# Performance work log

Measured on AMD Instinct MI355X. Metric: run time of the kernel, lower is better.

## Reference

```python
import jax, jax.numpy as jnp
import numpy as np

EMBED_DIM = 1024
NUM_HEADS = 16
HEAD_DIM = EMBED_DIM // NUM_HEADS


def layer_norm(x, gamma, beta, eps=1e-5):
    mu = jnp.mean(x, axis=-1, keepdims=True)
    var = jnp.var(x, axis=-1, keepdims=True)
    return (x - mu) * jax.lax.rsqrt(var + eps) * gamma + beta


def setup_inputs() -> dict:
    key = jax.random.key(0)
    ks = jax.random.split(key, 8)
    D = EMBED_DIM
    s = 1.0 / np.sqrt(D)
    x = jax.random.normal(ks[0], (2, 2048, D), dtype=jnp.float32)
    Wq = jax.random.uniform(ks[1], (D, D), jnp.float32, -s, s)
    Wk = jax.random.uniform(ks[2], (D, D), jnp.float32, -s, s)
    Wv = jax.random.uniform(ks[3], (D, D), jnp.float32, -s, s)
    W1 = jax.random.uniform(ks[4], (D, 4 * D), jnp.float32, -s, s)
    b1 = jnp.zeros((4 * D,), jnp.float32)
    W2 = jax.random.uniform(ks[5], (4 * D, D), jnp.float32, -1.0 / np.sqrt(4 * D), 1.0 / np.sqrt(4 * D))
    b2 = jnp.zeros((D,), jnp.float32)
    g1 = jnp.ones((D,), jnp.float32); be1 = jnp.zeros((D,), jnp.float32)
    g2 = jnp.ones((D,), jnp.float32); be2 = jnp.zeros((D,), jnp.float32)
    return {"x": x, "Wq": Wq, "Wk": Wk, "Wv": Wv, "W1": W1, "b1": b1,
            "W2": W2, "b2": b2, "g1": g1, "be1": be1, "g2": g2, "be2": be2}


def reference(x, Wq, Wk, Wv, W1, b1, W2, b2, g1, be1, g2, be2):
    B, S, D = x.shape
    H, Hd = NUM_HEADS, HEAD_DIM
    x_norm = layer_norm(x, g1, be1)
    # QKV projections (no bias), split into heads: [B, H, S, Hd]
    q = (x_norm @ Wq).reshape(B, S, H, Hd).transpose(0, 2, 1, 3)
    k = (x_norm @ Wk).reshape(B, S, H, Hd).transpose(0, 2, 1, 3)
    v = (x_norm @ Wv).reshape(B, S, H, Hd).transpose(0, 2, 1, 3)
    energy = jnp.einsum('bhqd,bhkd->bhqk', q, k)
    attn = jax.nn.softmax(energy / jnp.sqrt(jnp.float32(Hd)), axis=-1)
    out = jnp.einsum('bhqk,bhkd->bhqd', attn, v)
    attention = out.transpose(0, 2, 1, 3).reshape(B, S, D)
    x_res = attention + x
    x_norm2 = layer_norm(x_res, g2, be2)
    # Faithful quirk: FFN applied to x_res (not x_norm2)
    ffn_out = jax.nn.relu(x_res @ W1 + b1) @ W2 + b2
    return ffn_out + x_norm2
```

## Files before the change

kernel.cpp:

```cpp
#include <hip/hip_runtime.h>
#include <hip/hip_bf16.h>
#include <stdint.h>

typedef __hip_bfloat16 bf16;
typedef __attribute__((ext_vector_type(4))) float f32x4;
typedef __attribute__((ext_vector_type(8))) short s16x8;
typedef __attribute__((ext_vector_type(4))) short s16x4;

#define DEV static __device__ __forceinline__

DEV short f2bf(float f) {
  bf16 h = __float2bfloat16(f);
  short s;
  __builtin_memcpy(&s, &h, 2);
  return s;
}
DEV float bf2f(short s) {
  bf16 h;
  __builtin_memcpy(&h, &s, 2);
  return __bfloat162float(h);
}

__global__ __launch_bounds__(256) void transpose_cvt(
    const float* __restrict__ W, bf16* __restrict__ Wt, int K, int N)
{
  __shared__ float tile[32][33];
  const int n0 = blockIdx.x << 5;
  const int k0 = blockIdx.y << 5;
  const int tx = threadIdx.x & 31, ty = threadIdx.x >> 5;
#pragma unroll
  for (int i = 0; i < 4; ++i)
    tile[ty + i * 8][tx] = W[(size_t)(k0 + ty + i * 8) * N + n0 + tx];
  __syncthreads();
#pragma unroll
  for (int i = 0; i < 4; ++i)
    Wt[(size_t)(n0 + ty + i * 8) * K + k0 + tx] = __float2bfloat16(tile[tx][ty + i * 8]);
}

__global__ __launch_bounds__(256) void ln_bf16(
    const float* __restrict__ x, const float* __restrict__ g,
    const float* __restrict__ be, bf16* __restrict__ out)
{
  const int t = threadIdx.x;
  const size_t row = blockIdx.x;
  const float4 v = ((const float4*)(x + row * 1024))[t];
  float s = v.x + v.y + v.z + v.w;
  float ss = v.x * v.x + v.y * v.y + v.z * v.z + v.w * v.w;
#pragma unroll
  for (int off = 32; off > 0; off >>= 1) {
    s += __shfl_down(s, off);
    ss += __shfl_down(ss, off);
  }
  __shared__ float sh[8];
  const int wave = t >> 6, lane = t & 63;
  if (!lane) { sh[wave] = s; sh[4 + wave] = ss; }
  __syncthreads();
  s = sh[0] + sh[1] + sh[2] + sh[3];
  ss = sh[4] + sh[5] + sh[6] + sh[7];
  const float mean = s * (1.f / 1024.f);
  const float rstd = rsqrtf(ss * (1.f / 1024.f) - mean * mean + 1e-5f);
  const float4 gv = ((const float4*)g)[t];
  const float4 bv = ((const float4*)be)[t];
  s16x4 o;
  o[0] = f2bf((v.x - mean) * rstd * gv.x + bv.x);
  o[1] = f2bf((v.y - mean) * rstd * gv.y + bv.y);
  o[2] = f2bf((v.z - mean) * rstd * gv.z + bv.z);
  o[3] = f2bf((v.w - mean) * rstd * gv.w + bv.w);
  ((s16x4*)(out + row * 1024))[t] = o;
}

__global__ __launch_bounds__(256) void add_ln_bf16(
    const float* __restrict__ a, const float* __restrict__ x,
    const float* __restrict__ g, const float* __restrict__ be,
    bf16* __restrict__ xres, bf16* __restrict__ xnorm)
{
  const int t = threadIdx.x;
  const size_t row = blockIdx.x;
  const float4 av = ((const float4*)(a + row * 1024))[t];
  const float4 xv = ((const float4*)(x + row * 1024))[t];
  float4 v;
  v.x = av.x + xv.x; v.y = av.y + xv.y; v.z = av.z + xv.z; v.w = av.w + xv.w;
  float s = v.x + v.y + v.z + v.w;
  float ss = v.x * v.x + v.y * v.y + v.z * v.z + v.w * v.w;
#pragma unroll
  for (int off = 32; off > 0; off >>= 1) {
    s += __shfl_down(s, off);
    ss += __shfl_down(ss, off);
  }
  __shared__ float sh[8];
  const int wave = t >> 6, lane = t & 63;
  if (!lane) { sh[wave] = s; sh[4 + wave] = ss; }
  __syncthreads();
  s = sh[0] + sh[1] + sh[2] + sh[3];
  ss = sh[4] + sh[5] + sh[6] + sh[7];
  const float mean = s * (1.f / 1024.f);
  const float rstd = rsqrtf(ss * (1.f / 1024.f) - mean * mean + 1e-5f);
  const float4 gv = ((const float4*)g)[t];
  const float4 bv = ((const float4*)be)[t];
  s16x4 r, o;
  r[0] = f2bf(v.x); r[1] = f2bf(v.y); r[2] = f2bf(v.z); r[3] = f2bf(v.w);
  o[0] = f2bf((v.x - mean) * rstd * gv.x + bv.x);
  o[1] = f2bf((v.y - mean) * rstd * gv.y + bv.y);
  o[2] = f2bf((v.z - mean) * rstd * gv.z + bv.z);
  o[3] = f2bf((v.w - mean) * rstd * gv.w + bv.w);
  ((s16x4*)(xres + row * 1024))[t] = r;
  ((s16x4*)(xnorm + row * 1024))[t] = o;
}

__global__ __launch_bounds__(256) void ffn2_epi(
    const float* __restrict__ p0, float* __restrict__ out,
    const float* __restrict__ bias, const bf16* __restrict__ xn2)
{
  const int t = threadIdx.x;
  const size_t row = blockIdx.x;
  const float4 a = ((const float4*)(p0 + row * 1024))[t];
  const float4 b = ((const float4*)(out + row * 1024))[t];
  const float4 bv = ((const float4*)bias)[t];
  const s16x4 xv = ((const s16x4*)(xn2 + row * 1024))[t];
  float4 o;
  o.x = a.x + b.x + bv.x + bf2f(xv[0]);
  o.y = a.y + b.y + bv.y + bf2f(xv[1]);
  o.z = a.z + b.z + bv.z + bf2f(xv[2]);
  o.w = a.w + b.w + bv.w + bf2f(xv[3]);
  ((float4*)(out + row * 1024))[t] = o;
}

template <int EPI>
__global__ __launch_bounds__(256) void gemm_bt(
    const bf16* __restrict__ A, const bf16* __restrict__ Bt,
    void* __restrict__ C, const float* __restrict__ bias,
    const bf16* __restrict__ add_bf16, int M, int N, int K)
{
  __shared__ bf16 sA0[128 * 64];
  __shared__ bf16 sB0[128 * 64];
  __shared__ bf16 sA1[128 * 64];
  __shared__ bf16 sB1[128 * 64];
  const int tid = threadIdx.x;
  const int wave = tid >> 6, lane = tid & 63;
  const int fr = lane & 15, fg = lane >> 4;
  const int f7 = fr & 7;
  const int wr = wave >> 1, wc = wave & 1;
  const int nbx = N >> 7;
  int bid = blockIdx.x;
  if ((gridDim.x & 7) == 0) {
    const int cpx = gridDim.x >> 3;
    bid = (bid & 7) * cpx + (bid >> 3);
  }
  const int brow = (bid / nbx) << 7;
  const int bcol = (bid % nbx) << 7;

  f32x4 acc[4][4] = {};

  const int rsub = lane >> 3;
  const int cl = (lane & 7) ^ rsub;
  size_t ga[4], gb[4];
  int la[4];
#pragma unroll
  for (int j = 0; j < 4; ++j) {
    const int r = wave * 32 + j * 8;
    ga[j] = (size_t)(brow + r + rsub) * K + cl * 8;
    gb[j] = (size_t)(bcol + r + rsub) * K + cl * 8;
    la[j] = r * 64;
  }

#define GSTAGE(SA, SB, koff)                                                   \
  do {                                                                         \
    _Pragma("unroll")                                                          \
    for (int jj = 0; jj < 4; ++jj) {                                           \
      __builtin_amdgcn_global_load_lds(                                        \
          (const __attribute__((address_space(1))) uint32_t*)(A + ga[jj] + (koff)), \
          (__attribute__((address_space(3))) uint32_t*)(&SA[la[jj]]), 16, 0, 0);  \
      __builtin_amdgcn_global_load_lds(                                        \
          (const __attribute__((address_space(1))) uint32_t*)(Bt + gb[jj] + (koff)),\
          (__attribute__((address_space(3))) uint32_t*)(&SB[la[jj]]), 16, 0, 0);  \
    }                                                                          \
  } while (0)

#define COMPUTE(SA, SB)                                                        \
  do {                                                                         \
    s16x8 af[4][2], bfr[4][2];                                                 \
    _Pragma("unroll")                                                          \
    for (int m = 0; m < 4; ++m)                                                \
      _Pragma("unroll")                                                        \
      for (int kk = 0; kk < 2; ++kk)                                           \
        af[m][kk] = *(const s16x8*)(&SA[(wr * 64 + m * 16 + fr) * 64 +         \
                                        (((kk * 4 + fg) ^ f7) << 3)]);         \
    _Pragma("unroll")                                                          \
    for (int n = 0; n < 4; ++n)                                                \
      _Pragma("unroll")                                                        \
      for (int kk = 0; kk < 2; ++kk)                                           \
        bfr[n][kk] = *(const s16x8*)(&SB[(wc * 64 + n * 16 + fr) * 64 +        \
                                         (((kk * 4 + fg) ^ f7) << 3)]);        \
    _Pragma("unroll")                                                          \
    for (int kk = 0; kk < 2; ++kk)                                             \
      _Pragma("unroll")                                                        \
      for (int m = 0; m < 4; ++m)                                              \
        _Pragma("unroll")                                                      \
        for (int n = 0; n < 4; ++n)                                            \
          acc[m][n] = __builtin_amdgcn_mfma_f32_16x16x32_bf16(                 \
              af[m][kk], bfr[n][kk], acc[m][n], 0, 0, 0);                      \
  } while (0)

  GSTAGE(sA0, sB0, 0);
  __syncthreads();

  int kt = 0;
  for (;;) {
    if (kt + 64 < K) {
      GSTAGE(sA1, sB1, kt + 64);
      COMPUTE(sA0, sB0);
      __syncthreads();
    } else {
      COMPUTE(sA0, sB0);
      break;
    }
    kt += 64;
    if (kt + 64 < K) {
      GSTAGE(sA0, sB0, kt + 64);
      COMPUTE(sA1, sB1);
      __syncthreads();
    } else {
      COMPUTE(sA1, sB1);
      break;
    }
    kt += 64;
  }
#undef GSTAGE
#undef COMPUTE

  const int crow = brow + wr * 64;
  const int ccol = bcol + wc * 64;
#pragma unroll
  for (int m = 0; m < 4; ++m) {
#pragma unroll
    for (int n = 0; n < 4; ++n) {
      const int col = ccol + n * 16 + fr;
#pragma unroll
      for (int j = 0; j < 4; ++j) {
        const int row = crow + m * 16 + fg * 4 + j;
        float v = acc[m][n][j];
        if (EPI == 0) {
          ((bf16*)C)[(size_t)row * N + col] = __float2bfloat16(v);
        } else if (EPI == 1) {
          v += bias[col];
          v = fmaxf(v, 0.f);
          ((bf16*)C)[(size_t)row * N + col] = __float2bfloat16(v);
        } else {
          float a;
          {
            bf16 hb = add_bf16[(size_t)row * N + col];
            a = __bfloat162float(hb);
          }
          ((float*)C)[(size_t)row * N + col] = v + bias[col] + a;
        }
      }
    }
  }
}

__global__ __launch_bounds__(256) void gemm_splitk(
    const bf16* __restrict__ A, const bf16* __restrict__ Bt,
    float* __restrict__ P0, float* __restrict__ P1, int M, int N, int K, int KH)
{
  __shared__ bf16 sA0[128 * 64];
  __shared__ bf16 sB0[128 * 64];
  __shared__ bf16 sA1[128 * 64];
  __shared__ bf16 sB1[128 * 64];
  const int tid = threadIdx.x;
  const int wave = tid >> 6, lane = tid & 63;
  const int fr = lane & 15, fg = lane >> 4;
  const int f7 = fr & 7;
  const int wr = wave >> 1, wc = wave & 1;
  const int nbx = N >> 7;
  int bid = blockIdx.x;
  if ((gridDim.x & 7) == 0) {
    const int cpx = gridDim.x >> 3;
    bid = (bid & 7) * cpx + (bid >> 3);
  }
  const int brow = (bid / nbx) << 7;
  const int bcol = (bid % nbx) << 7;
  const int kbeg = blockIdx.y * KH;
  float* Cp = blockIdx.y ? P1 : P0;

  f32x4 acc[4][4] = {};

  const int rsub = lane >> 3;
  const int cl = (lane & 7) ^ rsub;
  size_t ga[4], gb[4];
  int la[4];
#pragma unroll
  for (int j = 0; j < 4; ++j) {
    const int r = wave * 32 + j * 8;
    ga[j] = (size_t)(brow + r + rsub) * K + cl * 8 + kbeg;
    gb[j] = (size_t)(bcol + r + rsub) * K + cl * 8 + kbeg;
    la[j] = r * 64;
  }

#define GSTAGE(SA, SB, koff)                                                   \
  do {                                                                         \
    _Pragma("unroll")                                                          \
    for (int jj = 0; jj < 4; ++jj) {                                           \
      __builtin_amdgcn_global_load_lds(                                        \
          (const __attribute__((address_space(1))) uint32_t*)(A + ga[jj] + (koff)), \
          (__attribute__((address_space(3))) uint32_t*)(&SA[la[jj]]), 16, 0, 0);  \
      __builtin_amdgcn_global_load_lds(                                        \
          (const __attribute__((address_space(1))) uint32_t*)(Bt + gb[jj] + (koff)),\
          (__attribute__((address_space(3))) uint32_t*)(&SB[la[jj]]), 16, 0, 0);  \
    }                                                                          \
  } while (0)

#define COMPUTE(SA, SB)                                                        \
  do {                                                                         \
    s16x8 af[4][2], bfr[4][2];                                                 \
    _Pragma("unroll")                                                          \
    for (int m = 0; m < 4; ++m)                                                \
      _Pragma("unroll")                                                        \
      for (int kk = 0; kk < 2; ++kk)                                           \
        af[m][kk] = *(const s16x8*)(&SA[(wr * 64 + m * 16 + fr) * 64 +         \
                                        (((kk * 4 + fg) ^ f7) << 3)]);         \
    _Pragma("unroll")                                                          \
    for (int n = 0; n < 4; ++n)                                                \
      _Pragma("unroll")                                                        \
      for (int kk = 0; kk < 2; ++kk)                                           \
        bfr[n][kk] = *(const s16x8*)(&SB[(wc * 64 + n * 16 + fr) * 64 +        \
                                         (((kk * 4 + fg) ^ f7) << 3)]);        \
    _Pragma("unroll")                                                          \
    for (int kk = 0; kk < 2; ++kk)                                             \
      _Pragma("unroll")                                                        \
      for (int m = 0; m < 4; ++m)                                              \
        _Pragma("unroll")                                                      \
        for (int n = 0; n < 4; ++n)                                            \
          acc[m][n] = __builtin_amdgcn_mfma_f32_16x16x32_bf16(                 \
              af[m][kk], bfr[n][kk], acc[m][n], 0, 0, 0);                      \
  } while (0)

  GSTAGE(sA0, sB0, 0);
  __syncthreads();

  int kt = 0;
  for (;;) {
    if (kt + 64 < KH) {
      GSTAGE(sA1, sB1, kt + 64);
      COMPUTE(sA0, sB0);
      __syncthreads();
    } else {
      COMPUTE(sA0, sB0);
      break;
    }
    kt += 64;
    if (kt + 64 < KH) {
      GSTAGE(sA0, sB0, kt + 64);
      COMPUTE(sA1, sB1);
      __syncthreads();
    } else {
      COMPUTE(sA1, sB1);
      break;
    }
    kt += 64;
  }
#undef GSTAGE
#undef COMPUTE

  const int crow = brow + wr * 64;
  const int ccol = bcol + wc * 64;
#pragma unroll
  for (int m = 0; m < 4; ++m) {
#pragma unroll
    for (int n = 0; n < 4; ++n) {
      const int col = ccol + n * 16 + fr;
#pragma unroll
      for (int j = 0; j < 4; ++j) {
        const int row = crow + m * 16 + fg * 4 + j;
        Cp[(size_t)row * N + col] = acc[m][n][j];
      }
    }
  }
}

template <int EPI>
__global__ __launch_bounds__(512) void gemm256_bt(
    const bf16* __restrict__ A, const bf16* __restrict__ Bt,
    void* __restrict__ C, const float* __restrict__ bias, int M, int N, int K)
{
  __shared__ bf16 sA0[256 * 64];
  __shared__ bf16 sB0[256 * 64];
  __shared__ bf16 sA1[256 * 64];
  __shared__ bf16 sB1[256 * 64];
  const int tid = threadIdx.x;
  const int wave = tid >> 6, lane = tid & 63;
  const int fr = lane & 15, fg = lane >> 4;
  const int f7 = fr & 7;
  const int wr = wave >> 2, wc = wave & 3;
  const int nbx = N >> 8;
  int bid = blockIdx.x;
  if ((gridDim.x & 7) == 0) {
    const int cpx = gridDim.x >> 3;
    bid = (bid & 7) * cpx + (bid >> 3);
  }
  const int brow = (bid / nbx) << 8;
  const int bcol = (bid % nbx) << 8;

  f32x4 acc[8][4] = {};

  const int rsub = lane >> 3;
  const int cl = (lane & 7) ^ rsub;
  size_t ga[4], gb[4];
  int la[4];
#pragma unroll
  for (int j = 0; j < 4; ++j) {
    const int r = j * 64 + wave * 8;
    ga[j] = (size_t)(brow + r + rsub) * K + cl * 8;
    gb[j] = (size_t)(bcol + r + rsub) * K + cl * 8;
    la[j] = r * 64;
  }

#define STG6(SA, SB, koff)                                                     \
  do {                                                                         \
    _Pragma("unroll")                                                          \
    for (int jj = 0; jj < 4; ++jj) {                                           \
      __builtin_amdgcn_global_load_lds(                                        \
          (const __attribute__((address_space(1))) uint32_t*)(A + ga[jj] + (koff)), \
          (__attribute__((address_space(3))) uint32_t*)(&SA[la[jj]]), 16, 0, 0);  \
      __builtin_amdgcn_global_load_lds(                                        \
          (const __attribute__((address_space(1))) uint32_t*)(Bt + gb[jj] + (koff)),\
          (__attribute__((address_space(3))) uint32_t*)(&SB[la[jj]]), 16, 0, 0);  \
    }                                                                          \
  } while (0)

#define CMP6(SA, SB)                                                           \
  do {                                                                         \
    s16x8 bfr[4][2];                                                           \
    _Pragma("unroll")                                                          \
    for (int n = 0; n < 4; ++n)                                                \
      _Pragma("unroll")                                                        \
      for (int kk = 0; kk < 2; ++kk)                                           \
        bfr[n][kk] = *(const s16x8*)(&SB[(wc * 64 + n * 16 + fr) * 64 +        \
                                         (((kk * 4 + fg) ^ f7) << 3)]);        \
    __builtin_amdgcn_s_setprio(1);                                             \
    _Pragma("unroll")                                                          \
    for (int m = 0; m < 8; ++m) {                                              \
      s16x8 afm[2];                                                            \
      _Pragma("unroll")                                                        \
      for (int kk = 0; kk < 2; ++kk)                                           \
        afm[kk] = *(const s16x8*)(&SA[(wr * 128 + m * 16 + fr) * 64 +          \
                                      (((kk * 4 + fg) ^ f7) << 3)]);           \
      _Pragma("unroll")                                                        \
      for (int kk = 0; kk < 2; ++kk)                                           \
        _Pragma("unroll")                                                      \
        for (int n = 0; n < 4; ++n)                                            \
          acc[m][n] = __builtin_amdgcn_mfma_f32_16x16x32_bf16(                 \
              afm[kk], bfr[n][kk], acc[m][n], 0, 0, 0);                        \
    }                                                                          \
    __builtin_amdgcn_s_setprio(0);                                             \
  } while (0)

  STG6(sA0, sB0, 0);

  int kt = 0;
  for (;;) {
    if (kt + 64 < K) {
      STG6(sA1, sB1, kt + 64);
      asm volatile("s_waitcnt vmcnt(8)" ::: "memory");
    } else {
      asm volatile("s_waitcnt vmcnt(0)" ::: "memory");
    }
    __builtin_amdgcn_s_barrier();
    __builtin_amdgcn_sched_barrier(0);
    CMP6(sA0, sB0);
    if (kt + 64 >= K) break;
    __builtin_amdgcn_s_barrier();
    __builtin_amdgcn_sched_barrier(0);
    kt += 64;
    if (kt + 64 < K) {
      STG6(sA0, sB0, kt + 64);
      asm volatile("s_waitcnt vmcnt(8)" ::: "memory");
    } else {
      asm volatile("s_waitcnt vmcnt(0)" ::: "memory");
    }
    __builtin_amdgcn_s_barrier();
    __builtin_amdgcn_sched_barrier(0);
    CMP6(sA1, sB1);
    if (kt + 64 >= K) break;
    __builtin_amdgcn_s_barrier();
    __builtin_amdgcn_sched_barrier(0);
    kt += 64;
  }
#undef STG6
#undef CMP6

  const int crow = brow + wr * 128;
  const int ccol = bcol + wc * 64;
#pragma unroll
  for (int m = 0; m < 8; ++m) {
#pragma unroll
    for (int n = 0; n < 4; ++n) {
      const int col = ccol + n * 16 + fr;
#pragma unroll
      for (int j = 0; j < 4; ++j) {
        const int row = crow + m * 16 + fg * 4 + j;
        float v = acc[m][n][j];
        if (EPI == 0) {
          ((bf16*)C)[(size_t)row * N + col] = __float2bfloat16(v);
        } else {
          v += bias[col];
          v = fmaxf(v, 0.f);
          ((bf16*)C)[(size_t)row * N + col] = __float2bfloat16(v);
        }
      }
    }
  }
}

__global__ __launch_bounds__(512, 4) void attn_fwd(
    const bf16* __restrict__ QK, const bf16* __restrict__ Vt,
    float* __restrict__ Out)
{
  const int LDK = 2048;
  const int qt = blockIdx.x;
  const int bh = blockIdx.y;
  const int b = bh >> 4, h = bh & 15;
  const int tid = threadIdx.x;
  const int wave = tid >> 6, lane = tid & 63;
  const int fr = lane & 15, fg = lane >> 4;
  const int f7 = fr & 7;

  const short* base = (const short*)QK + (size_t)b * 2048 * LDK;
  const short* Qp = base + h * 64;
  const short* Kp = base + 1024 + h * 64;
  const short* Vp = (const short*)Vt + (size_t)h * 64 * 4096 + b * 2048;
  const int q0 = qt * 128 + wave * 16;

  __shared__ short Kbuf0[64 * 64];
  __shared__ short Vbuf0[64 * 64];
  __shared__ short Kbuf1[64 * 64];
  __shared__ short Vbuf1[64 * 64];
  __shared__ short P_lds[8][16 * 72];
  short* Pw = P_lds[wave];

  const int rsub = lane >> 3;
  const int clog = (lane & 7) ^ rsub;
  const short* Ksrc = Kp + (size_t)(8 * wave + rsub) * LDK + clog * 8;
  const short* Vsrc = Vp + (size_t)(8 * wave + rsub) * 4096 + clog * 8;

  s16x8 qf0 = *(const s16x8*)(Qp + (size_t)(q0 + fr) * LDK + fg * 8);
  s16x8 qf1 = *(const s16x8*)(Qp + (size_t)(q0 + fr) * LDK + 32 + fg * 8);
#pragma unroll
  for (int i = 0; i < 8; ++i) {
    qf0[i] = f2bf(bf2f(qf0[i]) * 0.125f);
    qf1[i] = f2bf(bf2f(qf1[i]) * 0.125f);
  }

  f32x4 acc[4] = {};
  f32x4 mrow = {-1e30f, -1e30f, -1e30f, -1e30f};
  f32x4 lrow = {};

#define STAGE(KB, VB, koff)                                                    \
  do {                                                                         \
    __builtin_amdgcn_global_load_lds(                                          \
        (const __attribute__((address_space(1))) uint32_t*)(Ksrc + (size_t)(koff) * LDK), \
        (__attribute__((address_space(3))) uint32_t*)(&KB[wave * 512]),        \
        16, 0, 0);                                                             \
    __builtin_amdgcn_global_load_lds(                                          \
        (const __attribute__((address_space(1))) uint32_t*)(Vsrc + (koff)),    \
        (__attribute__((address_space(3))) uint32_t*)(&VB[wave * 512]),        \
        16, 0, 0);                                                             \
  } while (0)

#define ATTN_STEP(KB, VB)                                                      \
  do {                                                                         \
    f32x4 e[4];                                                                \
    __builtin_amdgcn_s_setprio(1);                                             \
    _Pragma("unroll")                                                          \
    for (int t = 0; t < 4; ++t) {                                              \
      const int ro = (t * 16 + fr) * 64;                                       \
      const s16x8 k0 = *(const s16x8*)(&KB[ro + ((fg ^ f7) << 3)]);            \
      const s16x8 k1 = *(const s16x8*)(&KB[ro + (((4 + fg) ^ f7) << 3)]);      \
      f32x4 z = {};                                                            \
      z = __builtin_amdgcn_mfma_f32_16x16x32_bf16(qf0, k0, z, 0, 0, 0);        \
      z = __builtin_amdgcn_mfma_f32_16x16x32_bf16(qf1, k1, z, 0, 0, 0);        \
      e[t] = z;                                                                \
    }                                                                          \
    __builtin_amdgcn_s_setprio(0);                                             \
    f32x4 lmx;                                                                 \
    _Pragma("unroll")                                                          \
    for (int j = 0; j < 4; ++j)                                                \
      lmx[j] = fmaxf(fmaxf(e[0][j], e[1][j]), fmaxf(e[2][j], e[3][j]));        \
    const bool need = (lmx[0] > mrow[0] + 8.f) | (lmx[1] > mrow[1] + 8.f) |    \
                      (lmx[2] > mrow[2] + 8.f) | (lmx[3] > mrow[3] + 8.f);     \
    if (__any(need)) {                                                         \
      f32x4 mx = lmx;                                                          \
      _Pragma("unroll")                                                        \
      for (int d = 1; d < 16; d <<= 1)                                         \
        _Pragma("unroll")                                                      \
        for (int j = 0; j < 4; ++j) mx[j] = fmaxf(mx[j], __shfl_xor(mx[j], d));\
      _Pragma("unroll")                                                        \
      for (int j = 0; j < 4; ++j) {                                            \
        const float mn = fmaxf(mrow[j], mx[j]);                                \
        const float al = __expf(mrow[j] - mn);                                 \
        lrow[j] *= al;                                                         \
        mrow[j] = mn;                                                          \
        _Pragma("unroll")                                                      \
        for (int nn = 0; nn < 4; ++nn) acc[nn][j] *= al;                       \
      }                                                                        \
    }                                                                          \
    _Pragma("unroll")                                                          \
    for (int j = 0; j < 4; ++j) {                                              \
      _Pragma("unroll")                                                        \
      for (int t = 0; t < 4; ++t) e[t][j] = __expf(e[t][j] - mrow[j]);         \
      lrow[j] += (e[0][j] + e[1][j]) + (e[2][j] + e[3][j]);                    \
    }                                                                          \
    _Pragma("unroll")                                                          \
    for (int t = 0; t < 4; ++t)                                                \
      _Pragma("unroll")                                                        \
      for (int j = 0; j < 4; ++j)                                              \
        Pw[(fg * 4 + j) * 72 + t * 16 + fr] = f2bf(e[t][j]);                   \
    const s16x8 pf0 = *(const s16x8*)(Pw + fr * 72 + fg * 8);                  \
    const s16x8 pf1 = *(const s16x8*)(Pw + fr * 72 + 32 + fg * 8);             \
    __builtin_amdgcn_s_setprio(1);                                             \
    _Pragma("unroll")                                                          \
    for (int nn = 0; nn < 4; ++nn) {                                           \
      const int ro = (nn * 16 + fr) * 64;                                      \
      const s16x8 vf0 = *(const s16x8*)(&VB[ro + ((fg ^ f7) << 3)]);           \
      const s16x8 vf1 = *(const s16x8*)(&VB[ro + (((4 + fg) ^ f7) << 3)]);     \
      acc[nn] = __builtin_amdgcn_mfma_f32_16x16x32_bf16(pf0, vf0, acc[nn], 0, 0, 0); \
      acc[nn] = __builtin_amdgcn_mfma_f32_16x16x32_bf16(pf1, vf1, acc[nn], 0, 0, 0); \
    }                                                                          \
    __builtin_amdgcn_s_setprio(0);                                             \
  } while (0)

  STAGE(Kbuf0, Vbuf0, 0);

  for (int kt = 0; kt < 2048; kt += 128) {
    STAGE(Kbuf1, Vbuf1, kt + 64);
    asm volatile("s_waitcnt vmcnt(2)" ::: "memory");
    __builtin_amdgcn_s_barrier();
    __builtin_amdgcn_sched_barrier(0);
    ATTN_STEP(Kbuf0, Vbuf0);
    __builtin_amdgcn_s_barrier();
    __builtin_amdgcn_sched_barrier(0);
    if (kt + 128 < 2048) {
      STAGE(Kbuf0, Vbuf0, kt + 128);
      asm volatile("s_waitcnt vmcnt(2)" ::: "memory");
    } else {
      asm volatile("s_waitcnt vmcnt(0)" ::: "memory");
    }
    __builtin_amdgcn_s_barrier();
    __builtin_amdgcn_sched_barrier(0);
    ATTN_STEP(Kbuf1, Vbuf1);
    __builtin_amdgcn_s_barrier();
    __builtin_amdgcn_sched_barrier(0);
  }
#undef STAGE
#undef ATTN_STEP

#pragma unroll
  for (int d = 1; d < 16; d <<= 1)
#pragma unroll
    for (int j = 0; j < 4; ++j) lrow[j] += __shfl_xor(lrow[j], d);
  f32x4 inv;
#pragma unroll
  for (int j = 0; j < 4; ++j) inv[j] = 1.0f / lrow[j];
  float* outp = Out + (size_t)(b * 2048 + q0) * 1024 + h * 64;
#pragma unroll
  for (int nn = 0; nn < 4; ++nn)
#pragma unroll
    for (int j = 0; j < 4; ++j)
      outp[(size_t)(fg * 4 + j) * 1024 + nn * 16 + fr] = acc[nn][j] * inv[j];
}

extern "C" void kernel_launch(void* const* d_in, const int* in_sizes, int n_in,
                              void* d_out, int out_size, void* d_ws, size_t ws_size,
                              hipStream_t stream)
{
  const float* x   = (const float*)d_in[0];
  const float* Wq  = (const float*)d_in[1];
  const float* Wk  = (const float*)d_in[2];
  const float* Wv  = (const float*)d_in[3];
  const float* W1  = (const float*)d_in[4];
  const float* b1  = (const float*)d_in[5];
  const float* W2  = (const float*)d_in[6];
  const float* b2  = (const float*)d_in[7];
  const float* g1  = (const float*)d_in[8];
  const float* be1 = (const float*)d_in[9];
  const float* g2  = (const float*)d_in[10];
  const float* be2 = (const float*)d_in[11];
  float* out = (float*)d_out;

  const int M = 4096, D = 1024, DF = 4096;

  bf16* Wqk_t = (bf16*)d_ws;
  bf16* Wv_t  = Wqk_t + (size_t)2048 * 1024;
  bf16* W1t   = Wv_t + (size_t)1024 * 1024;
  bf16* W2t   = W1t + (size_t)4096 * 1024;
  bf16* big   = W2t + (size_t)4096 * 1024;
  bf16* QK    = big;
  bf16* Vt    = big + (size_t)8 * 1024 * 1024;
  bf16* hbuf  = big;
  char* p2    = (char*)(big + (size_t)16 * 1024 * 1024);
  bf16* xnorm = (bf16*)p2;
  float* attnO = (float*)p2;
  float* part0 = (float*)p2;
  char* p3    = p2 + (size_t)M * D * sizeof(float);
  bf16* xres  = (bf16*)p3;
  bf16* xnorm2 = xres + (size_t)M * D;

  transpose_cvt<<<dim3(32, 32), 256, 0, stream>>>(Wq, Wqk_t, D, D);
  transpose_cvt<<<dim3(32, 32), 256, 0, stream>>>(Wk, Wqk_t + (size_t)D * D, D, D);
  transpose_cvt<<<dim3(32, 32), 256, 0, stream>>>(Wv, Wv_t, D, D);
  transpose_cvt<<<dim3(128, 32), 256, 0, stream>>>(W1, W1t, D, DF);
  transpose_cvt<<<dim3(32, 128), 256, 0, stream>>>(W2, W2t, DF, D);
  ln_bf16<<<M, 256, 0, stream>>>(x, g1, be1, xnorm);
  gemm_bt<0><<<(M / 128) * (2048 / 128), 256, 0, stream>>>(
      xnorm, Wqk_t, QK, nullptr, nullptr, M, 2048, D);
  gemm_bt<0><<<(D / 128) * (M / 128), 256, 0, stream>>>(
      Wv_t, xnorm, Vt, nullptr, nullptr, D, M, D);
  attn_fwd<<<dim3(16, 32), 512, 0, stream>>>(QK, Vt, attnO);
  add_ln_bf16<<<M, 256, 0, stream>>>(attnO, x, g2, be2, xres, xnorm2);
  gemm256_bt<1><<<(M / 256) * (DF / 256), 512, 0, stream>>>(
      xres, W1t, hbuf, b1, M, DF, D);
  gemm_splitk<<<dim3((M / 128) * (D / 128), 2), 256, 0, stream>>>(
      hbuf, W2t, part0, out, M, D, DF, DF / 2);
  ffn2_epi<<<M, 256, 0, stream>>>(part0, out, b2, xnorm2);
}
```

Before: 227.1 us.

## Process two 16-row query subtiles per wave in attention to reuse K/V fragments

Each attention wave now handles 32 query rows (two 16-row subtiles) instead of 16, so every K and V fragment read from shared memory feeds two sets of MFMAs. The block covers 256 queries and the grid halves to 256 blocks, with launch bounds relaxed to 2 blocks per CU to allow more registers. This cuts LDS traffic and global K/V staging per query. The cost is more register pressure and fewer blocks to fill the CUs.

Result: slower. 234.0 us (+3.0%).

```diff
diff --git a/kernel.cpp b/kernel.cpp
--- a/kernel.cpp
+++ b/kernel.cpp
@@ -511,7 +511,7 @@
   }
 }
 
-__global__ __launch_bounds__(512, 4) void attn_fwd(
+__global__ __launch_bounds__(512, 2) void attn_fwd(
     const bf16* __restrict__ QK, const bf16* __restrict__ Vt,
     float* __restrict__ Out)
 {
@@ -528,13 +528,13 @@
   const short* Qp = base + h * 64;
   const short* Kp = base + 1024 + h * 64;
   const short* Vp = (const short*)Vt + (size_t)h * 64 * 4096 + b * 2048;
-  const int q0 = qt * 128 + wave * 16;
+  const int q0 = qt * 256 + wave * 32;
 
   __shared__ short Kbuf0[64 * 64];
   __shared__ short Vbuf0[64 * 64];
   __shared__ short Kbuf1[64 * 64];
   __shared__ short Vbuf1[64 * 64];
-  __shared__ short P_lds[8][16 * 72];
+  __shared__ short P_lds[8][32 * 72];
   short* Pw = P_lds[wave];
 
   const int rsub = lane >> 3;
@@ -542,17 +542,23 @@
   const short* Ksrc = Kp + (size_t)(8 * wave + rsub) * LDK + clog * 8;
   const short* Vsrc = Vp + (size_t)(8 * wave + rsub) * 4096 + clog * 8;
 
-  s16x8 qf0 = *(const s16x8*)(Qp + (size_t)(q0 + fr) * LDK + fg * 8);
-  s16x8 qf1 = *(const s16x8*)(Qp + (size_t)(q0 + fr) * LDK + 32 + fg * 8);
-#pragma unroll
-  for (int i = 0; i < 8; ++i) {
-    qf0[i] = f2bf(bf2f(qf0[i]) * 0.125f);
-    qf1[i] = f2bf(bf2f(qf1[i]) * 0.125f);
-  }
-
-  f32x4 acc[4] = {};
-  f32x4 mrow = {-1e30f, -1e30f, -1e30f, -1e30f};
-  f32x4 lrow = {};
+  s16x8 qf[2][2];
+#pragma unroll
+  for (int s = 0; s < 2; ++s) {
+    qf[s][0] = *(const s16x8*)(Qp + (size_t)(q0 + s * 16 + fr) * LDK + fg * 8);
+    qf[s][1] = *(const s16x8*)(Qp + (size_t)(q0 + s * 16 + fr) * LDK + 32 + fg * 8);
+#pragma unroll
+    for (int i = 0; i < 8; ++i) {
+      qf[s][0][i] = f2bf(bf2f(qf[s][0][i]) * 0.125f);
+      qf[s][1][i] = f2bf(bf2f(qf[s][1][i]) * 0.125f);
+    }
+  }
+
+  f32x4 acc[2][4] = {};
+  f32x4 mrow[2], lrow[2] = {};
+#pragma unroll
+  for (int s = 0; s < 2; ++s)
+    mrow[s] = f32x4{-1e30f, -1e30f, -1e30f, -1e30f};
 
 #define STAGE(KB, VB, koff)                                                    \
   do {                                                                         \
@@ -568,64 +574,80 @@
 
 #define ATTN_STEP(KB, VB)                                                      \
   do {                                                                         \
-    f32x4 e[4];                                                                \
-    __builtin_amdgcn_s_setprio(1);                                             \
+                        \
+    s16x8 kf[4][2];                                                            \
     _Pragma("unroll")                                                          \
     for (int t = 0; t < 4; ++t) {                                              \
       const int ro = (t * 16 + fr) * 64;                                       \
-      const s16x8 k0 = *(const s16x8*)(&KB[ro + ((fg ^ f7) << 3)]);            \
-      const s16x8 k1 = *(const s16x8*)(&KB[ro + (((4 + fg) ^ f7) << 3)]);      \
-      f32x4 z = {};                                                            \
-      z = __builtin_amdgcn_mfma_f32_16x16x32_bf16(qf0, k0, z, 0, 0, 0);        \
-      z = __builtin_amdgcn_mfma_f32_16x16x32_bf16(qf1, k1, z, 0, 0, 0);        \
-      e[t] = z;                                                                \
+      kf[t][0] = *(const s16x8*)(&KB[ro + ((fg ^ f7) << 3)]);                  \
+      kf[t][1] = *(const s16x8*)(&KB[ro + (((4 + fg) ^ f7) << 3)]);            \
     }                                                                          \
-    __builtin_amdgcn_s_setprio(0);                                             \
-    f32x4 lmx;                                                                 \
-    _Pragma("unroll")                                                          \
-    for (int j = 0; j < 4; ++j)                                                \
-      lmx[j] = fmaxf(fmaxf(e[0][j], e[1][j]), fmaxf(e[2][j], e[3][j]));        \
-    const bool need = (lmx[0] > mrow[0] + 8.f) | (lmx[1] > mrow[1] + 8.f) |    \
-                      (lmx[2] > mrow[2] + 8.f) | (lmx[3] > mrow[3] + 8.f);     \
-    if (__any(need)) {                                                         \
-      f32x4 mx = lmx;                                                          \
-      _Pragma("unroll")                                                        \
-      for (int d = 1; d < 16; d <<= 1)                                         \
+    _Pragma("unroll")                                                          \
+    for (int s = 0; s < 2; ++s) {                                              \
+      f32x4 e[4];                                                              \
+      __builtin_amdgcn_s_setprio(1);                                           \
+      _Pragma("unroll")                                                        \
+      for (int t = 0; t < 4; ++t) {                                            \
+        f32x4 z = {};                                                          \
+        z = __builtin_amdgcn_mfma_f32_16x16x32_bf16(qf[s][0], kf[t][0], z, 0, 0, 0); \
+        z = __builtin_amdgcn_mfma_f32_16x16x32_bf16(qf[s][1], kf[t][1], z, 0, 0, 0); \
+        e[t] = z;                                                              \
+      }                                                                        \
+      __builtin_amdgcn_s_setprio(0);                                           \
+      f32x4 lmx;                                                               \
+      _Pragma("unroll")                                                        \
+      for (int j = 0; j < 4; ++j)                                              \
+        lmx[j] = fmaxf(fmaxf(e[0][j], e[1][j]), fmaxf(e[2][j], e[3][j]));      \
+      const bool need = (lmx[0] > mrow[s][0] + 8.f) | (lmx[1] > mrow[s][1] + 8.f) | \
+                        (lmx[2] > mrow[s][2] + 8.f) | (lmx[3] > mrow[s][3] + 8.f);  \
+      if (__any(need)) {                                                       \
+        f32x4 mx = lmx;                                                        \
         _Pragma("unroll")                                                      \
-        for (int j = 0; j < 4; ++j) mx[j] = fmaxf(mx[j], __shfl_xor(mx[j], d));\
+        for (int d = 1; d < 16; d <<= 1)                                       \
+          _Pragma("unroll")                                                    \
+          for (int j = 0; j < 4; ++j) mx[j] = fmaxf(mx[j], __shfl_xor(mx[j], d)); \
+        _Pragma("unroll")                                                      \
+        for (int j = 0; j < 4; ++j) {                                          \
+          const float mn = fmaxf(mrow[s][j], mx[j]);                           \
+          const float al = __expf(mrow[s][j] - mn);                            \
+          lrow[s][j] *= al;                                                    \
+          mrow[s][j] = mn;                                                     \
+          _Pragma("unroll")                                                    \
+          for (int nn = 0; nn < 4; ++nn) acc[s][nn][j] *= al;                  \
+        }                                                                      \
+      }                                                                        \
       _Pragma("unroll")                                                        \
       for (int j = 0; j < 4; ++j) {                                            \
-        const float mn = fmaxf(mrow[j], mx[j]);                                \
-        const float al = __expf(mrow[j] - mn);                                 \
-        lrow[j] *= al;                                                         \
-        mrow[j] = mn;                                                          \
         _Pragma("unroll")                                                      \
-        for (int nn = 0; nn < 4; ++nn) acc[nn][j] *= al;                       \
+        for (int t = 0; t < 4; ++t) e[t][j] = __expf(e[t][j] - mrow[s][j]);    \
+        lrow[s][j] += (e[0][j] + e[1][j]) + (e[2][j] + e[3][j]);               \
       }                                                                        \
+      _Pragma("unroll")                                                        \
+      for (int t = 0; t < 4; ++t)                                              \
+        _Pragma("unroll")                                                      \
+        for (int j = 0; j < 4; ++j)                                            \
+          Pw[(s * 16 + fg * 4 + j) * 72 + t * 16 + fr] = f2bf(e[t][j]);        \
     }                                                                          \
-    _Pragma("unroll")                                                          \
-    for (int j = 0; j < 4; ++j) {                                              \
-      _Pragma("unroll")                                                        \
-      for (int t = 0; t < 4; ++t) e[t][j] = __expf(e[t][j] - mrow[j]);         \
-      lrow[j] += (e[0][j] + e[1][j]) + (e[2][j] + e[3][j]);                    \
-    }                                                                          \
-    _Pragma("unroll")                                                          \
-    for (int t = 0; t < 4; ++t)                                                \
-      _Pragma("unroll")                                                        \
-      for (int j = 0; j < 4; ++j)                                              \
-        Pw[(fg * 4 + j) * 72 + t * 16 + fr] = f2bf(e[t][j]);                   \
-    const s16x8 pf0 = *(const s16x8*)(Pw + fr * 72 + fg * 8);                  \
-    const s16x8 pf1 = *(const s16x8*)(Pw + fr * 72 + 32 + fg * 8);             \
-    __builtin_amdgcn_s_setprio(1);                                             \
+                        \
+    s16x8 vf[4][2];                                                            \
     _Pragma("unroll")                                                          \
     for (int nn = 0; nn < 4; ++nn) {                                           \
       const int ro = (nn * 16 + fr) * 64;                                      \
-      const s16x8 vf0 = *(const s16x8*)(&VB[ro + ((fg ^ f7) << 3)]);           \
-      const s16x8 vf1 = *(const s16x8*)(&VB[ro + (((4 + fg) ^ f7) << 3)]);     \
-      acc[nn] = __builtin_amdgcn_mfma_f32_16x16x32_bf16(pf0, vf0, acc[nn], 0, 0, 0); \
-      acc[nn] = __builtin_amdgcn_mfma_f32_16x16x32_bf16(pf1, vf1, acc[nn], 0, 0, 0); \
+      vf[nn][0] = *(const s16x8*)(&VB[ro + ((fg ^ f7) << 3)]);                 \
+      vf[nn][1] = *(const s16x8*)(&VB[ro + (((4 + fg) ^ f7) << 3)]);           \
     }                                                                          \
-    __builtin_amdgcn_s_setprio(0);                                             \
+    _Pragma("unroll")                                                          \
+    for (int s = 0; s < 2; ++s) {                                              \
+      const s16x8 pf0 = *(const s16x8*)(Pw + (s * 16 + fr) * 72 + fg * 8);     \
+      const s16x8 pf1 = *(const s16x8*)(Pw + (s * 16 + fr) * 72 + 32 + fg * 8);\
+      __builtin_amdgcn_s_setprio(1);                                           \
+      _Pragma("unroll")                                                        \
+      for (int nn = 0; nn < 4; ++nn) {                                         \
+        acc[s][nn] = __builtin_amdgcn_mfma_f32_16x16x32_bf16(pf0, vf[nn][0], acc[s][nn], 0, 0, 0); \
+        acc[s][nn] = __builtin_amdgcn_mfma_f32_16x16x32_bf16(pf1, vf[nn][1], acc[s][nn], 0, 0, 0); \
+      }                                                                        \
+      __builtin_amdgcn_s_setprio(0);                                           \
+    }                                                                          \
   } while (0)
 
   STAGE(Kbuf0, Vbuf0, 0);
@@ -654,18 +676,21 @@
 #undef ATTN_STEP
 
 #pragma unroll
-  for (int d = 1; d < 16; d <<= 1)
-#pragma unroll
-    for (int j = 0; j < 4; ++j) lrow[j] += __shfl_xor(lrow[j], d);
-  f32x4 inv;
-#pragma unroll
-  for (int j = 0; j < 4; ++j) inv[j] = 1.0f / lrow[j];
-  float* outp = Out + (size_t)(b * 2048 + q0) * 1024 + h * 64;
-#pragma unroll
-  for (int nn = 0; nn < 4; ++nn)
-#pragma unroll
-    for (int j = 0; j < 4; ++j)
-      outp[(size_t)(fg * 4 + j) * 1024 + nn * 16 + fr] = acc[nn][j] * inv[j];
+  for (int s = 0; s < 2; ++s) {
+#pragma unroll
+    for (int d = 1; d < 16; d <<= 1)
+#pragma unroll
+      for (int j = 0; j < 4; ++j) lrow[s][j] += __shfl_xor(lrow[s][j], d);
+    f32x4 inv;
+#pragma unroll
+    for (int j = 0; j < 4; ++j) inv[j] = 1.0f / lrow[s][j];
+    float* outp = Out + (size_t)(b * 2048 + q0 + s * 16) * 1024 + h * 64;
+#pragma unroll
+    for (int nn = 0; nn < 4; ++nn)
+#pragma unroll
+      for (int j = 0; j < 4; ++j)
+        outp[(size_t)(fg * 4 + j) * 1024 + nn * 16 + fr] = acc[s][nn][j] * inv[j];
+  }
 }
 
 extern "C" void kernel_launch(void* const* d_in, const int* in_sizes, int n_in,
@@ -714,7 +739,7 @@
       xnorm, Wqk_t, QK, nullptr, nullptr, M, 2048, D);
   gemm_bt<0><<<(D / 128) * (M / 128), 256, 0, stream>>>(
       Wv_t, xnorm, Vt, nullptr, nullptr, D, M, D);
-  attn_fwd<<<dim3(16, 32), 512, 0, stream>>>(QK, Vt, attnO);
+  attn_fwd<<<dim3(8, 32), 512, 0, stream>>>(QK, Vt, attnO);
   add_ln_bf16<<<M, 256, 0, stream>>>(attnO, x, g2, be2, xres, xnorm2);
   gemm256_bt<1><<<(M / 256) * (DF / 256), 512, 0, stream>>>(
       xres, W1t, hbuf, b1, M, DF, D);
```
